# Optimization experiments

Hardware: AMD Instinct MI355X
Metric: run time of the kernel (lower is better)

Reference implementation:

```python
import jax, jax.numpy as jnp
import numpy as np

VOCAB = 50257
K = 10  # accuracy_slack_size


def setup_inputs() -> dict:
    key = jax.random.key(0)
    k1, k2, k3, k4 = jax.random.split(key, 4)
    logits = jax.random.normal(k1, (4, 2048, 512), dtype=jnp.float32)
    target = jax.random.randint(k2, (4, 2048), 0, VOCAB, dtype=jnp.int64 if jax.config.jax_enable_x64 else jnp.int32)
    mask = jax.random.randint(k3, (4, 2048), 0, 2, dtype=jnp.int32)
    W = jax.random.normal(k4, (512, VOCAB), dtype=jnp.float32) * 0.02
    b = jnp.zeros((VOCAB,), dtype=jnp.float32)
    return {"logits": logits, "target": target, "mask": mask, "W": W, "b": b}


def reference(logits, target, mask, W, b):
    N = logits.shape[0] * logits.shape[1]
    x = logits.reshape(N, logits.shape[-1])            # [N, d]
    # sampled_softmax.log_prob: full log-softmax over vocab
    logp = jax.nn.log_softmax(x @ W + b, axis=-1)      # [N, V]
    _, words = jax.lax.top_k(logp, K)                  # [N, K] indices
    tgt = target.reshape(-1)                           # [N]
    msk = mask.reshape(-1).astype(jnp.float32)         # [N]
    # vectorized membership: is target among top-K predictions?
    hit = jnp.any(words == tgt[:, None], axis=1).astype(jnp.float32)
    counter = jnp.sum(hit * msk)
    all_counter = jnp.sum(msk)
    return jnp.array([counter / all_counter])
```

## Files before the change

### kernel.cpp

```cpp
#include <hip/hip_runtime.h>
#include <stdint.h>

#define V_VOCAB 50257
#define V_PAD   51200
#define NROWS   8192
#define DIM     512
#define KTOP    10
#define ACH     16

typedef __attribute__((ext_vector_type(8))) short  short8;
typedef __attribute__((ext_vector_type(4))) float  f32x4;
typedef __attribute__((ext_vector_type(4))) int    i32x4;
typedef __attribute__((ext_vector_type(2))) unsigned int u32x2;

struct Ctrl { int mc; int namb; int hits; int pad_; };

#define OFF_WT8    0ULL
#define SZ_WT8     26214400ULL
#define OFF_XQ8    (OFF_WT8 + SZ_WT8)
#define SZ_XQ8     4194304ULL
#define OFF_BPAD   (OFF_XQ8 + SZ_XQ8)
#define SZ_COL     (51200ULL*4)
#define OFF_SW8    (OFF_BPAD + SZ_COL)
#define OFF_W1     (OFF_SW8 + SZ_COL)
#define OFF_IVW    (OFF_W1 + SZ_COL)
#define OFF_ROWIDX (OFF_IVW + SZ_COL)
#define OFF_SXR    (OFF_ROWIDX + 32768ULL)
#define OFF_X1     (OFF_SXR + 32768ULL)
#define OFF_RMETA  (OFF_X1 + 32768ULL)
#define OFF_COUNTS (OFF_RMETA + 131072ULL)
#define OFF_AMB    (OFF_COUNTS + 32768ULL)
#define OFF_CTRL   (OFF_AMB + 32768ULL)
#define OFF_RK     (OFF_CTRL + 16ULL)
#define OFF_SST    (OFF_RK + 32768ULL)

#define GLOAD16(gp, lp) __builtin_amdgcn_global_load_lds( \
    (const __attribute__((address_space(1))) unsigned int*)(gp), \
    (__attribute__((address_space(3))) unsigned int*)(lp), 16, 0, 0)

__global__ void k_prep(const int* __restrict__ mask, const float* __restrict__ b,
                       float* __restrict__ bpad, int* __restrict__ rowidx,
                       Ctrl* __restrict__ ctrl) {
  int i = blockIdx.x * 256 + threadIdx.x;
  if (i < V_PAD) bpad[i] = (i < V_VOCAB) ? b[i] : -1e30f;
  if (i < NROWS && mask[i] != 0) {
    int p = atomicAdd(&ctrl->mc, 1);
    rowidx[p] = i;
  }
}

__global__ void k_wstat(const float* __restrict__ W, float* __restrict__ sw8,
                        float* __restrict__ w1, float* __restrict__ invw) {
  const int j = blockIdx.x * 256 + threadIdx.x;
  if (j >= V_PAD) return;
  if (j >= V_VOCAB) { sw8[j] = 1.f; w1[j] = 0.f; invw[j] = 0.f; return; }
  float am = 0.f, s1 = 0.f;
  for (int k = 0; k < DIM; ++k) {
    float v = fabsf(W[(size_t)k * V_VOCAB + j]);
    am = fmaxf(am, v);
    s1 += v;
  }
  sw8[j] = (am > 0.f) ? am / 126.f : 1.f;
  invw[j] = (am > 0.f) ? 126.f / am : 0.f;
  w1[j] = s1;
}

__global__ void k_twt8(const float* __restrict__ W, const float* __restrict__ invw,
                       signed char* __restrict__ Wt8) {
  __shared__ float lt[64][65];
  const int vbase = blockIdx.x * 64;
  const int kbase = blockIdx.y * 64;
  const int tid = threadIdx.x;
  const int krow = tid >> 6;
  const int col  = tid & 63;
  const int v    = vbase + col;
#pragma unroll
  for (int rr = 0; rr < 16; ++rr) {
    int kl = krow + rr * 4;
    float val = (v < V_VOCAB) ? W[(size_t)(kbase + kl) * V_VOCAB + v] : 0.0f;
    lt[kl][col] = val;
  }
  __syncthreads();
  const int vr = tid >> 3;
  const int kc = tid & 7;
#pragma unroll
  for (int p = 0; p < 2; ++p) {
    const int vl = p * 32 + vr;
    const float inv = invw[vbase + vl];
    unsigned int lo = 0, hi = 0;
#pragma unroll
    for (int j = 0; j < 4; ++j) {
      int q = (int)rintf(lt[kc * 8 + j][vl] * inv);
      lo |= ((unsigned int)(q & 255)) << (8 * j);
    }
#pragma unroll
    for (int j = 0; j < 4; ++j) {
      int q = (int)rintf(lt[kc * 8 + 4 + j][vl] * inv);
      hi |= ((unsigned int)(q & 255)) << (8 * j);
    }
    u32x2 t; t.x = lo; t.y = hi;
    *(u32x2*)(Wt8 + (size_t)(vbase + vl) * DIM + kbase + kc * 8) = t;
  }
}

__global__ void k_xq(const float* __restrict__ x, const int* __restrict__ rowidx,
                     const Ctrl* __restrict__ ctrl, signed char* __restrict__ Xq8,
                     float* __restrict__ sxr, float* __restrict__ x1) {
  const int wid = threadIdx.x >> 6, lane = threadIdx.x & 63;
  const int i = blockIdx.x * 4 + wid;
  const int mc = ctrl->mc;
  if (i >= mc) {
    u32x2 z; z.x = 0; z.y = 0;
    *(u32x2*)(Xq8 + (size_t)i * DIM + lane * 8) = z;
    if (lane == 0) { sxr[i] = 1.f; x1[i] = 0.f; }
    return;
  }
  const float* src = x + (size_t)rowidx[i] * DIM + lane * 8;
  float v[8];
  float am = 0.f, s1 = 0.f;
#pragma unroll
  for (int j = 0; j < 8; ++j) {
    v[j] = src[j];
    float a = fabsf(v[j]);
    am = fmaxf(am, a);
    s1 += a;
  }
#pragma unroll
  for (int d = 1; d < 64; d <<= 1) {
    am = fmaxf(am, __shfl_xor(am, d, 64));
    s1 += __shfl_xor(s1, d, 64);
  }
  const float sx  = (am > 0.f) ? am / 126.f : 1.f;
  const float inv = (am > 0.f) ? 126.f / am : 0.f;
  unsigned int lo = 0, hi = 0;
#pragma unroll
  for (int j = 0; j < 4; ++j) {
    int q = (int)rintf(v[j] * inv);
    lo |= ((unsigned int)(q & 255)) << (8 * j);
  }
#pragma unroll
  for (int j = 0; j < 4; ++j) {
    int q = (int)rintf(v[4 + j] * inv);
    hi |= ((unsigned int)(q & 255)) << (8 * j);
  }
  u32x2 t; t.x = lo; t.y = hi;
  *(u32x2*)(Xq8 + (size_t)i * DIM + lane * 8) = t;
  if (lane == 0) { sxr[i] = sx; x1[i] = s1; }
}

__global__ void k_that8(const signed char* __restrict__ Xq8,
                        const signed char* __restrict__ Wt8,
                        const float* __restrict__ bpad, const float* __restrict__ sw8,
                        const float* __restrict__ w1,
                        const float* __restrict__ sxr, const float* __restrict__ x1,
                        const int* __restrict__ rowidx, const int* __restrict__ target,
                        const Ctrl* __restrict__ ctrl, f32x4* __restrict__ rmeta) {
  const int wid = threadIdx.x >> 6, lane = threadIdx.x & 63;
  const int i = blockIdx.x * 4 + wid;
  const int mc = ctrl->mc;
  if (i >= mc) {
    if (lane == 0) { f32x4 rm; rm.x = 1.f; rm.y = 1e30f; rm.z = 0.f; rm.w = 0.f; rmeta[i] = rm; }
    return;
  }
  const int tg = target[rowidx[i]];
  u32x2 xq = *(const u32x2*)(Xq8 + (size_t)i * DIM + lane * 8);
  u32x2 wq = *(const u32x2*)(Wt8 + (size_t)tg * DIM + lane * 8);
  int d = 0;
#pragma unroll
  for (int j = 0; j < 4; ++j)
    d += (int)((signed char)(xq.x >> (8 * j))) * (int)((signed char)(wq.x >> (8 * j)));
#pragma unroll
  for (int j = 0; j < 4; ++j)
    d += (int)((signed char)(xq.y >> (8 * j))) * (int)((signed char)(wq.y >> (8 * j)));
#pragma unroll
  for (int dd = 1; dd < 64; dd <<= 1) d += __shfl_xor(d, dd, 64);
  if (lane == 0) {
    const float sx = sxr[i], sw = sw8[tg], xl1 = x1[i];
    f32x4 rm;
    rm.x = sx;
    rm.y = fmaf((float)d, sx * sw, bpad[tg]);
    rm.z = 0.5005f * (sx * w1[tg] + sw * xl1) + 128.5f * (sx * sw)
           + 1e-3f;
    rm.w = fmaf(128.5f, sx, 0.5005f * xl1);
    rmeta[i] = rm;
  }
}

__launch_bounds__(256, 3)
__global__ void k_count8(const signed char* __restrict__ Xq8,
                         const signed char* __restrict__ Wt8,
                         const float* __restrict__ bpad, const float* __restrict__ sw8,
                         const float* __restrict__ w1, const f32x4* __restrict__ rmeta,
                         const Ctrl* __restrict__ ctrl, unsigned int* __restrict__ counts) {
  const int mc = ctrl->mc;
  const int lin = blockIdx.x;
  const int xcd = lin & 7;
  const int idx = lin >> 3;
  const int mt  = xcd * 4 + (idx & 3);
  const int nt  = idx >> 2;
  const int nbase = nt * 128;

  __shared__ char lds[32768];

  const int tid  = threadIdx.x;
  const int lane = tid & 63;
  const int w    = tid >> 6;
  const int wr   = w >> 1;
  const int wc   = w & 1;

  const char* Bg = (const char*)Wt8 + (size_t)nbase * 512;
  const int r8   = tid >> 3;
  const int sws  = ((tid & 7) ^ (r8 & 7)) * 16;
  const int dst0 = tid * 16;

  const int fr = lane & 15;
  const int fq = lane >> 4;
  const int p0 = ((fq) ^ (fr & 7)) * 16;
  const int p1 = ((4 + fq) ^ (fr & 7)) * 16;

#define STAGE(Ag, kt) do {                                                     \
    const size_t _kb = (size_t)(kt) * 128;                                     \
    _Pragma("unroll") for (int _c = 0; _c < 4; ++_c)                           \
      GLOAD16((Ag) + (size_t)(_c * 32 + r8) * 512 + _kb + sws,                 \
              lds + _c * 4096 + dst0);                                         \
    _Pragma("unroll") for (int _c = 0; _c < 4; ++_c)                           \
      GLOAD16(Bg + (size_t)(_c * 32 + r8) * 512 + _kb + sws,                   \
              lds + 16384 + _c * 4096 + dst0);                                 \
  } while (0)

#define KTILE() do {                                                           \
    _Pragma("unroll") for (int _ks = 0; _ks < 2; ++_ks) {                      \
      const int _p = _ks ? p1 : p0;                                            \
      i32x4 a4[4], b4[4];                                                      \
      _Pragma("unroll") for (int _i = 0; _i < 4; ++_i)                         \
        a4[_i] = *(const i32x4*)(lds + (wr * 64 + _i * 16 + fr) * 128 + _p);   \
      _Pragma("unroll") for (int _i = 0; _i < 4; ++_i)                         \
        b4[_i] = *(const i32x4*)(lds + 16384 +                                 \
                                 (wc * 64 + _i * 16 + fr) * 128 + _p);         \
      __builtin_amdgcn_s_setprio(1);                                           \
      _Pragma("unroll") for (int _m = 0; _m < 4; ++_m)                         \
      _Pragma("unroll") for (int _n = 0; _n < 4; ++_n)                         \
        acc[_m][_n] = __builtin_amdgcn_mfma_i32_16x16x64_i8(                   \
            a4[_m], b4[_n], acc[_m][_n], 0, 0, 0);                             \
      __builtin_amdgcn_s_setprio(0);                                           \
    }                                                                          \
  } while (0)

  i32x4 acc[4][4];

  float bv[4], swc[4], w1c[4];
#pragma unroll
  for (int ni = 0; ni < 4; ++ni) {
    const int c = nbase + wc * 64 + ni * 16 + fr;
    bv[ni] = bpad[c]; swc[ni] = sw8[c]; w1c[ni] = w1[c];
  }

  for (int mb = mt * 128; mb < mc; mb += 4096) {
    const char* Ag = (const char*)Xq8 + (size_t)mb * 512;
#pragma unroll
    for (int a = 0; a < 4; ++a)
#pragma unroll
      for (int c = 0; c < 4; ++c) acc[a][c] = (i32x4)0;

#pragma unroll
    for (int kt = 0; kt < 4; ++kt) {
      STAGE(Ag, kt);
      __syncthreads();
      KTILE();
      __syncthreads();
    }

#pragma unroll
    for (int mi = 0; mi < 4; ++mi) {
#pragma unroll
      for (int r = 0; r < 4; ++r) {
        const int m = mb + wr * 64 + mi * 16 + fq * 4 + r;
        const f32x4 rm = rmeta[m];
        const float arr = 0.5005f * rm.x;
        unsigned int p = 0;
#pragma unroll
        for (int ni = 0; ni < 4; ++ni) {
          const float s  = fmaf((float)acc[mi][ni][r], rm.x * swc[ni], bv[ni]);
          const float mm = fmaf(arr, w1c[ni], fmaf(rm.w, swc[ni], rm.z));
          p += (s > rm.y - mm) ? 1u : 0u;
          p += (s > rm.y + mm) ? (1u << 16) : 0u;
        }
        int pi = (int)p;
#pragma unroll
        for (int d = 1; d < 16; d <<= 1) pi += __shfl_xor(pi, d, 64);
        if ((lane & 15) == 0) atomicAdd(&counts[m], (unsigned int)pi);
      }
    }
  }
#undef STAGE
#undef KTILE
}

__global__ void k_decide(const unsigned int* __restrict__ counts,
                         Ctrl* __restrict__ ctrl, int* __restrict__ amb) {
  const int i = blockIdx.x * 256 + threadIdx.x;
  if (i >= ctrl->mc) return;
  const unsigned int c = counts[i];
  const unsigned int lo = c & 0xFFFFu, hi = c >> 16;
  if (lo <= KTOP - 1) { atomicAdd(&ctrl->hits, 1); }
  else if (hi >= KTOP) {  }
  else { int p = atomicAdd(&ctrl->namb, 1); amb[p] = i; }
}

__global__ void k_fixt(const float* __restrict__ x, const float* __restrict__ W,
                       const float* __restrict__ b, const int* __restrict__ rowidx,
                       const int* __restrict__ target, const int* __restrict__ amb,
                       const Ctrl* __restrict__ ctrl, float* __restrict__ sst) {
  const int a = blockIdx.x * 64 + threadIdx.x;
  if (a >= ctrl->namb) return;
  const int n = rowidx[amb[a]];
  const int tg = target[n];
  float st = 0.f;
  for (int k = 0; k < DIM; ++k)
    st = fmaf(x[(size_t)n * DIM + k], W[(size_t)k * V_VOCAB + tg], st);
  sst[a] = st + b[tg];
}

__global__ void k_fixscan(const float* __restrict__ x, const float* __restrict__ W,
                          const float* __restrict__ b, const int* __restrict__ rowidx,
                          const int* __restrict__ target, const int* __restrict__ amb,
                          const float* __restrict__ sst, const Ctrl* __restrict__ ctrl,
                          int* __restrict__ rk) {
  __shared__ float sx[ACH][DIM];
  const int j = blockIdx.x * 256 + threadIdx.x;
  const int namb = ctrl->namb;
  const float bj = (j < V_VOCAB) ? b[j] : 0.f;
  for (int base = 0; base < namb; base += ACH) {
    __syncthreads();
    for (int t = threadIdx.x; t < ACH * DIM / 4; t += 256) {
      const int a  = t / (DIM / 4);
      const int kk = (t % (DIM / 4)) * 4;
      f32x4 v = (f32x4)0.f;
      if (base + a < namb) {
        const int n = rowidx[amb[base + a]];
        v = *(const f32x4*)(x + (size_t)n * DIM + kk);
      }
      *(f32x4*)(&sx[a][kk]) = v;
    }
    __syncthreads();
    if (j >= V_VOCAB) continue;
    float s[ACH];
#pragma unroll
    for (int a = 0; a < ACH; ++a) s[a] = 0.f;
    for (int k = 0; k < DIM; ++k) {
      const float wv = W[(size_t)k * V_VOCAB + j];
#pragma unroll
      for (int a = 0; a < ACH; ++a) s[a] = fmaf(sx[a][k], wv, s[a]);
    }
#pragma unroll
    for (int a = 0; a < ACH; ++a) {
      if (base + a < namb) {
        const int tg = target[rowidx[amb[base + a]]];
        const float sc = s[a] + bj;
        const float st = sst[base + a];
        if (sc > st || (sc == st && j < tg)) atomicAdd(&rk[base + a], 1);
      }
    }
  }
}

__global__ void k_fixdec(const int* __restrict__ rk, Ctrl* __restrict__ ctrl) {
  const int a = blockIdx.x * 256 + threadIdx.x;
  if (a < ctrl->namb && rk[a] <= KTOP - 1) atomicAdd(&ctrl->hits, 1);
}

__global__ void k_final(const Ctrl* __restrict__ ctrl, float* __restrict__ out) {
  out[0] = (float)ctrl->hits / (float)ctrl->mc;
}

extern "C" void kernel_launch(void* const* d_in, const int* in_sizes, int n_in,
                              void* d_out, int out_size, void* d_ws, size_t ws_size,
                              hipStream_t stream) {
  const float* x      = (const float*)d_in[0];
  const int*   target = (const int*)d_in[1];
  const int*   mask   = (const int*)d_in[2];
  const float* W      = (const float*)d_in[3];
  const float* b      = (const float*)d_in[4];
  float* out = (float*)d_out;

  char* ws = (char*)d_ws;
  signed char*    Wt8    = (signed char*)(ws + OFF_WT8);
  signed char*    Xq8    = (signed char*)(ws + OFF_XQ8);
  float*          bpad   = (float*)(ws + OFF_BPAD);
  float*          sw8    = (float*)(ws + OFF_SW8);
  float*          w1     = (float*)(ws + OFF_W1);
  float*          invw   = (float*)(ws + OFF_IVW);
  int*            rowidx = (int*)(ws + OFF_ROWIDX);
  float*          sxr    = (float*)(ws + OFF_SXR);
  float*          x1     = (float*)(ws + OFF_X1);
  f32x4*          rmeta  = (f32x4*)(ws + OFF_RMETA);
  unsigned int*   counts = (unsigned int*)(ws + OFF_COUNTS);
  int*            amb    = (int*)(ws + OFF_AMB);
  Ctrl*           ctrl   = (Ctrl*)(ws + OFF_CTRL);
  int*            rk     = (int*)(ws + OFF_RK);
  float*          sst    = (float*)(ws + OFF_SST);

  hipMemsetAsync(ws + OFF_COUNTS, 0, 32768 + 32768 + 16 + 32768, stream);

  k_prep   <<<200, 256, 0, stream>>>(mask, b, bpad, rowidx, ctrl);
  k_wstat  <<<200, 256, 0, stream>>>(W, sw8, w1, invw);
  k_twt8   <<<dim3(800, 8), 256, 0, stream>>>(W, invw, Wt8);
  k_xq     <<<2048, 256, 0, stream>>>(x, rowidx, ctrl, Xq8, sxr, x1);
  k_that8  <<<2048, 256, 0, stream>>>(Xq8, Wt8, bpad, sw8, w1, sxr, x1,
                                      rowidx, target, ctrl, rmeta);
  k_count8 <<<12800, 256, 0, stream>>>(Xq8, Wt8, bpad, sw8, w1, rmeta,
                                       ctrl, counts);
  k_decide <<<32, 256, 0, stream>>>(counts, ctrl, amb);
  k_fixt   <<<128, 64, 0, stream>>>(x, W, b, rowidx, target, amb, ctrl, sst);
  k_fixscan<<<197, 256, 0, stream>>>(x, W, b, rowidx, target, amb, sst, ctrl, rk);
  k_fixdec <<<32, 256, 0, stream>>>(rk, ctrl);
  k_final  <<<1, 1, 0, stream>>>(ctrl, out);
}
```

Before: 445.3 us.

## Fuse x-quantize with target-logit kernel, parallelize W stats, trim GEMM syncs

Merges the activation quantization and target-score kernels so the quantized row is used straight from registers, dropping the sxr/x1 intermediates and one launch. Splits the per-column W statistics over four waves with an LDS reduction, giving 800 blocks instead of 200, and moves the bias padding into that kernel. In the int8 count GEMM it removes the s_setprio hints and skips the final barrier when no further M iteration follows. Together these target launch overhead, the latency of the serial 512-step column loop, and barrier cost, at the price of more complex kernels.

```diff
diff --git a/kernel.cpp b/kernel.cpp
--- a/kernel.cpp
+++ b/kernel.cpp
@@ -25,9 +25,7 @@
 #define OFF_W1     (OFF_SW8 + SZ_COL)
 #define OFF_IVW    (OFF_W1 + SZ_COL)
 #define OFF_ROWIDX (OFF_IVW + SZ_COL)
-#define OFF_SXR    (OFF_ROWIDX + 32768ULL)
-#define OFF_X1     (OFF_SXR + 32768ULL)
-#define OFF_RMETA  (OFF_X1 + 32768ULL)
+#define OFF_RMETA  (OFF_ROWIDX + 32768ULL)
 #define OFF_COUNTS (OFF_RMETA + 131072ULL)
 #define OFF_AMB    (OFF_COUNTS + 32768ULL)
 #define OFF_CTRL   (OFF_AMB + 32768ULL)
@@ -38,31 +36,48 @@
     (const __attribute__((address_space(1))) unsigned int*)(gp), \
     (__attribute__((address_space(3))) unsigned int*)(lp), 16, 0, 0)
 
-__global__ void k_prep(const int* __restrict__ mask, const float* __restrict__ b,
-                       float* __restrict__ bpad, int* __restrict__ rowidx,
-                       Ctrl* __restrict__ ctrl) {
+__global__ void k_prep2(const int* __restrict__ mask, int* __restrict__ rowidx,
+                        Ctrl* __restrict__ ctrl) {
   int i = blockIdx.x * 256 + threadIdx.x;
-  if (i < V_PAD) bpad[i] = (i < V_VOCAB) ? b[i] : -1e30f;
   if (i < NROWS && mask[i] != 0) {
     int p = atomicAdd(&ctrl->mc, 1);
     rowidx[p] = i;
   }
 }
 
-__global__ void k_wstat(const float* __restrict__ W, float* __restrict__ sw8,
-                        float* __restrict__ w1, float* __restrict__ invw) {
-  const int j = blockIdx.x * 256 + threadIdx.x;
-  if (j >= V_PAD) return;
-  if (j >= V_VOCAB) { sw8[j] = 1.f; w1[j] = 0.f; invw[j] = 0.f; return; }
+__global__ void k_wstat2(const float* __restrict__ W, const float* __restrict__ b,
+                         float* __restrict__ sw8, float* __restrict__ w1,
+                         float* __restrict__ invw, float* __restrict__ bpad) {
+  __shared__ float redm[4][64];
+  __shared__ float reds[4][64];
+  const int tid = threadIdx.x;
+  const int c   = tid & 63;
+  const int kq  = tid >> 6;
+  const int j   = blockIdx.x * 64 + c;
   float am = 0.f, s1 = 0.f;
-  for (int k = 0; k < DIM; ++k) {
-    float v = fabsf(W[(size_t)k * V_VOCAB + j]);
-    am = fmaxf(am, v);
-    s1 += v;
-  }
-  sw8[j] = (am > 0.f) ? am / 126.f : 1.f;
-  invw[j] = (am > 0.f) ? 126.f / am : 0.f;
-  w1[j] = s1;
+  if (j < V_VOCAB) {
+    const float* p = W + (size_t)(kq * 128) * V_VOCAB + j;
+#pragma unroll 4
+    for (int k = 0; k < 128; ++k) {
+      float v = fabsf(p[(size_t)k * V_VOCAB]);
+      am = fmaxf(am, v);
+      s1 += v;
+    }
+  }
+  redm[kq][c] = am; reds[kq][c] = s1;
+  __syncthreads();
+  if (kq == 0) {
+    am = fmaxf(fmaxf(redm[0][c], redm[1][c]), fmaxf(redm[2][c], redm[3][c]));
+    s1 = reds[0][c] + reds[1][c] + reds[2][c] + reds[3][c];
+    if (j < V_VOCAB) {
+      sw8[j]  = (am > 0.f) ? am / 126.f : 1.f;
+      invw[j] = (am > 0.f) ? 126.f / am : 0.f;
+      w1[j]   = s1;
+      bpad[j] = b[j];
+    } else {
+      sw8[j] = 1.f; invw[j] = 0.f; w1[j] = 0.f; bpad[j] = -1e30f;
+    }
+  }
 }
 
 __global__ void k_twt8(const float* __restrict__ W, const float* __restrict__ invw,
@@ -103,19 +118,25 @@
   }
 }
 
-__global__ void k_xq(const float* __restrict__ x, const int* __restrict__ rowidx,
-                     const Ctrl* __restrict__ ctrl, signed char* __restrict__ Xq8,
-                     float* __restrict__ sxr, float* __restrict__ x1) {
+__global__ void k_xqt(const float* __restrict__ x, const int* __restrict__ rowidx,
+                      const int* __restrict__ target,
+                      const signed char* __restrict__ Wt8,
+                      const float* __restrict__ bpad, const float* __restrict__ sw8,
+                      const float* __restrict__ w1,
+                      const Ctrl* __restrict__ ctrl,
+                      signed char* __restrict__ Xq8, f32x4* __restrict__ rmeta) {
   const int wid = threadIdx.x >> 6, lane = threadIdx.x & 63;
   const int i = blockIdx.x * 4 + wid;
   const int mc = ctrl->mc;
   if (i >= mc) {
     u32x2 z; z.x = 0; z.y = 0;
     *(u32x2*)(Xq8 + (size_t)i * DIM + lane * 8) = z;
-    if (lane == 0) { sxr[i] = 1.f; x1[i] = 0.f; }
+    if (lane == 0) { f32x4 rm; rm.x = 1.f; rm.y = 1e30f; rm.z = 0.f; rm.w = 0.f; rmeta[i] = rm; }
     return;
   }
-  const float* src = x + (size_t)rowidx[i] * DIM + lane * 8;
+  const int n  = rowidx[i];
+  const int tg = target[n];
+  const float* src = x + (size_t)n * DIM + lane * 8;
   float v[8];
   float am = 0.f, s1 = 0.f;
 #pragma unroll
@@ -145,43 +166,25 @@
   }
   u32x2 t; t.x = lo; t.y = hi;
   *(u32x2*)(Xq8 + (size_t)i * DIM + lane * 8) = t;
-  if (lane == 0) { sxr[i] = sx; x1[i] = s1; }
-}
-
-__global__ void k_that8(const signed char* __restrict__ Xq8,
-                        const signed char* __restrict__ Wt8,
-                        const float* __restrict__ bpad, const float* __restrict__ sw8,
-                        const float* __restrict__ w1,
-                        const float* __restrict__ sxr, const float* __restrict__ x1,
-                        const int* __restrict__ rowidx, const int* __restrict__ target,
-                        const Ctrl* __restrict__ ctrl, f32x4* __restrict__ rmeta) {
-  const int wid = threadIdx.x >> 6, lane = threadIdx.x & 63;
-  const int i = blockIdx.x * 4 + wid;
-  const int mc = ctrl->mc;
-  if (i >= mc) {
-    if (lane == 0) { f32x4 rm; rm.x = 1.f; rm.y = 1e30f; rm.z = 0.f; rm.w = 0.f; rmeta[i] = rm; }
-    return;
-  }
-  const int tg = target[rowidx[i]];
-  u32x2 xq = *(const u32x2*)(Xq8 + (size_t)i * DIM + lane * 8);
+
   u32x2 wq = *(const u32x2*)(Wt8 + (size_t)tg * DIM + lane * 8);
   int d = 0;
 #pragma unroll
   for (int j = 0; j < 4; ++j)
-    d += (int)((signed char)(xq.x >> (8 * j))) * (int)((signed char)(wq.x >> (8 * j)));
+    d += (int)((signed char)(lo >> (8 * j))) * (int)((signed char)(wq.x >> (8 * j)));
 #pragma unroll
   for (int j = 0; j < 4; ++j)
-    d += (int)((signed char)(xq.y >> (8 * j))) * (int)((signed char)(wq.y >> (8 * j)));
+    d += (int)((signed char)(hi >> (8 * j))) * (int)((signed char)(wq.y >> (8 * j)));
 #pragma unroll
   for (int dd = 1; dd < 64; dd <<= 1) d += __shfl_xor(d, dd, 64);
   if (lane == 0) {
-    const float sx = sxr[i], sw = sw8[tg], xl1 = x1[i];
+    const float sw = sw8[tg];
     f32x4 rm;
     rm.x = sx;
     rm.y = fmaf((float)d, sx * sw, bpad[tg]);
-    rm.z = 0.5005f * (sx * w1[tg] + sw * xl1) + 128.5f * (sx * sw)
+    rm.z = 0.5005f * (sx * w1[tg] + sw * s1) + 128.5f * (sx * sw)
            + 1e-3f;
-    rm.w = fmaf(128.5f, sx, 0.5005f * xl1);
+    rm.w = fmaf(128.5f, sx, 0.5005f * s1);
     rmeta[i] = rm;
   }
 }
@@ -237,12 +240,10 @@
       _Pragma("unroll") for (int _i = 0; _i < 4; ++_i)                         \
         b4[_i] = *(const i32x4*)(lds + 16384 +                                 \
                                  (wc * 64 + _i * 16 + fr) * 128 + _p);         \
-      __builtin_amdgcn_s_setprio(1);                                           \
       _Pragma("unroll") for (int _m = 0; _m < 4; ++_m)                         \
       _Pragma("unroll") for (int _n = 0; _n < 4; ++_n)                         \
         acc[_m][_n] = __builtin_amdgcn_mfma_i32_16x16x64_i8(                   \
             a4[_m], b4[_n], acc[_m][_n], 0, 0, 0);                             \
-      __builtin_amdgcn_s_setprio(0);                                           \
     }                                                                          \
   } while (0)
 
@@ -267,7 +268,8 @@
       STAGE(Ag, kt);
       __syncthreads();
       KTILE();
-      __syncthreads();
+      if (kt < 3 || mb + 4096 < mc)
+        __syncthreads();
     }
 
 #pragma unroll
@@ -391,8 +393,6 @@
   float*          w1     = (float*)(ws + OFF_W1);
   float*          invw   = (float*)(ws + OFF_IVW);
   int*            rowidx = (int*)(ws + OFF_ROWIDX);
-  float*          sxr    = (float*)(ws + OFF_SXR);
-  float*          x1     = (float*)(ws + OFF_X1);
   f32x4*          rmeta  = (f32x4*)(ws + OFF_RMETA);
   unsigned int*   counts = (unsigned int*)(ws + OFF_COUNTS);
   int*            amb    = (int*)(ws + OFF_AMB);
@@ -402,12 +402,11 @@
 
   hipMemsetAsync(ws + OFF_COUNTS, 0, 32768 + 32768 + 16 + 32768, stream);
 
-  k_prep   <<<200, 256, 0, stream>>>(mask, b, bpad, rowidx, ctrl);
-  k_wstat  <<<200, 256, 0, stream>>>(W, sw8, w1, invw);
+  k_prep2  <<<32, 256, 0, stream>>>(mask, rowidx, ctrl);
+  k_wstat2 <<<800, 256, 0, stream>>>(W, b, sw8, w1, invw, bpad);
   k_twt8   <<<dim3(800, 8), 256, 0, stream>>>(W, invw, Wt8);
-  k_xq     <<<2048, 256, 0, stream>>>(x, rowidx, ctrl, Xq8, sxr, x1);
-  k_that8  <<<2048, 256, 0, stream>>>(Xq8, Wt8, bpad, sw8, w1, sxr, x1,
-                                      rowidx, target, ctrl, rmeta);
+  k_xqt    <<<2048, 256, 0, stream>>>(x, rowidx, target, Wt8, bpad, sw8, w1,
+                                      ctrl, Xq8, rmeta);
   k_count8 <<<12800, 256, 0, stream>>>(Xq8, Wt8, bpad, sw8, w1, rmeta,
                                        ctrl, counts);
   k_decide <<<32, 256, 0, stream>>>(counts, ctrl, amb);
```

New measurement: 463.2 us. +4.0%, slower.
